# Kernel tuning notes

Measured on AMD Instinct MI355X. Metric: run time of the kernel, lower is better.

## Reference

```python
import jax, jax.numpy as jnp
import numpy as np

D, H, B = 512, 8, 64
NF, NO = 16384, 8192
EPS = 1e-5


def _ln(x):
    m = jnp.mean(x, axis=-1, keepdims=True)
    v = jnp.mean((x - m) ** 2, axis=-1, keepdims=True)
    return (x - m) / jnp.sqrt(v + EPS)


def setup_inputs() -> dict:
    key = jax.random.key(0)
    ks = jax.random.split(key, 16)
    s = 1.0 / np.sqrt(D)
    inp = {
        "hf": jax.random.normal(ks[0], (NF, D), jnp.float32),
        "ho": jax.random.normal(ks[1], (NO, D), jnp.float32),
        "ps": jax.random.normal(ks[2], (B, D), jnp.float32),
        "face_batch": jnp.sort(jax.random.randint(ks[3], (NF,), 0, B)),
        "obj_batch": jnp.sort(jax.random.randint(ks[4], (NO,), 0, B)),
        "Wq": jax.random.normal(ks[5], (D, D), jnp.float32) * s,
        "bq": jnp.zeros((D,), jnp.float32),
        "Wk": jax.random.normal(ks[6], (D, D), jnp.float32) * s,
        "bk": jnp.zeros((D,), jnp.float32),
        "Wv": jax.random.normal(ks[7], (D, D), jnp.float32) * s,
        "bv": jnp.zeros((D,), jnp.float32),
        "Wo": jax.random.normal(ks[8], (D, D), jnp.float32) * s,
        "bo": jnp.zeros((D,), jnp.float32),
        "Wg": jax.random.normal(ks[9], (D, D), jnp.float32) * s,
        "bg": jnp.full((D,), -1.0, jnp.float32),  # init.constant_(bias, -1.0)
        "alpha": jax.random.normal(ks[10], (D,), jnp.float32) * 0.1,
    }
    return inp


def reference(hf, ho, ps, face_batch, obj_batch, Wq, bq, Wk, bk, Wv, bv, Wo, bo, Wg, bg, alpha):
    dh = D // H
    nodes = jnp.concatenate([hf, ho], axis=0)            # (N, D)
    seg = jnp.concatenate([face_batch, obj_batch], 0)    # (N,)
    N = nodes.shape[0]

    # single-query cross-attention done as ragged/segment attention
    # (identical math to padded MHA with key_padding_mask)
    q = (ps @ Wq + bq).reshape(B, H, dh)                 # (B, H, dh)
    k = (nodes @ Wk + bk).reshape(N, H, dh)
    v = (nodes @ Wv + bv).reshape(N, H, dh)

    scores = jnp.einsum("nhd,nhd->nh", k, q[seg]) / np.sqrt(dh)   # (N, H)
    mx = jax.ops.segment_max(scores, seg, num_segments=B)          # (B, H)
    e = jnp.exp(scores - mx[seg])                                  # (N, H)
    denom = jax.ops.segment_sum(e, seg, num_segments=B)            # (B, H)
    num = jax.ops.segment_sum(e[:, :, None] * v, seg, num_segments=B)  # (B, H, dh)
    attn = (num / denom[:, :, None]).reshape(B, D)
    attn_out = attn @ Wo + bo

    fs = _ln(ps + attn_out)                               # (B, D)
    gate = jax.nn.sigmoid(hf @ Wg + bg)                   # (NF, D)
    signal = alpha * fs[face_batch]                       # (NF, D)
    hf_new = _ln(hf + gate * signal)
    return hf_new, fs
```

## Files before the change

### kernel.cpp

```cpp
#include <hip/hip_runtime.h>
#include <hip/hip_bf16.h>
#include <math.h>

constexpr int D  = 512;
constexpr int H  = 8;
constexpr int DH = 64;
constexpr int B  = 64;
constexpr int NF = 16384;
constexpr int NO = 8192;
constexpr int NT = NF + NO;
constexpr float EPS = 1e-5f;
constexpr float LOG2E = 1.4426950408889634f;

constexpr int PREP_PK   = 512;
constexpr int PREP_BND  = PREP_PK;
constexpr int PREP_WG0  = PREP_BND + 1;
constexpr int PREP_CVT0 = PREP_WG0 + 256;
constexpr int CVT_BLOCKS = NT * D / 2048;
constexpr int PREP_TOTAL = PREP_CVT0 + CVT_BLOCKS;

typedef short short8 __attribute__((ext_vector_type(8)));
typedef float f32x4 __attribute__((ext_vector_type(4)));
typedef unsigned short ushort;
typedef ushort ushort8v __attribute__((ext_vector_type(8)));

__device__ __forceinline__ ushort f2bf(float f) {
  unsigned int x = __float_as_uint(f);
  x += 0x7FFF + ((x >> 16) & 1);
  return (ushort)(x >> 16);
}
__device__ __forceinline__ float bf2f(ushort u) {
  return __uint_as_float(((unsigned int)u) << 16);
}
__device__ __forceinline__ float fast_exp(float x) {
  return __builtin_amdgcn_exp2f(x * LOG2E);
}
__device__ __forceinline__ float fast_sigmoid(float z) {
  return __builtin_amdgcn_rcpf(1.0f + __builtin_amdgcn_exp2f(-z * LOG2E));
}
__device__ __forceinline__ short8 cvt8(float4 f0, float4 f1) {
  union { short8 v; __hip_bfloat162 h[4]; } u;
  u.h[0] = __float22bfloat162_rn(float2{f0.x, f0.y});
  u.h[1] = __float22bfloat162_rn(float2{f0.z, f0.w});
  u.h[2] = __float22bfloat162_rn(float2{f1.x, f1.y});
  u.h[3] = __float22bfloat162_rn(float2{f1.z, f1.w});
  return u.v;
}
__device__ __forceinline__ void gll16(const void* g, void* l) {
  __builtin_amdgcn_global_load_lds(
      (const __attribute__((address_space(1))) void*)g,
      (__attribute__((address_space(3))) void*)l, 16, 0, 0);
}

__global__ __launch_bounds__(256) void k_prep(const float* __restrict__ ps,
                                              const float* __restrict__ Wq,
                                              const float* __restrict__ bq,
                                              const float* __restrict__ Wk,
                                              const float* __restrict__ bk,
                                              const float* __restrict__ Wg,
                                              const float* __restrict__ hf,
                                              const float* __restrict__ ho,
                                              const int* __restrict__ fb,
                                              const int* __restrict__ ob,
                                              float* __restrict__ Pk,
                                              float* __restrict__ qbk,
                                              ushort* __restrict__ Wgt,
                                              ushort* __restrict__ nodesb,
                                              int* __restrict__ fstart,
                                              int* __restrict__ ostart) {
  __shared__ float shm[1056];
  const int bid = blockIdx.x, t = threadIdx.x;
  if (bid < PREP_PK) {
    const int b = bid >> 3, h = bid & 7;
    for (int i = t; i < D; i += 256) shm[i] = ps[(size_t)b * D + i];
    __syncthreads();
    {
      const int j = t >> 2, eq = t & 3;
      const int col = h * 64 + j;
      float acc = 0.f;
      const float* wp = Wq + (size_t)(eq * 128) * D + col;
      #pragma unroll 8
      for (int e = 0; e < 128; ++e) acc += shm[eq * 128 + e] * wp[(size_t)e * D];
      acc += __shfl_xor(acc, 1); acc += __shfl_xor(acc, 2);
      if (eq == 0) shm[512 + j] = acc + bq[col];
    }
    __syncthreads();
    for (int e = t; e < D; e += 256) {
      float acc = 0.f;
      #pragma unroll 8
      for (int j = 0; j < DH; ++j) acc += Wk[(size_t)e * D + h * DH + j] * shm[512 + j];
      Pk[((size_t)b * H + h) * D + e] = acc;
    }
    if (t == 0) {
      float s = 0.f;
      for (int j = 0; j < DH; ++j) s += bk[h * DH + j] * shm[512 + j];
      qbk[b * H + h] = s;
    }
  } else if (bid == PREP_BND) {
    if (t <= B) {
      int lo = 0, hi = NF;
      while (lo < hi) { int mid = (lo + hi) >> 1; if (fb[mid] < t) lo = mid + 1; else hi = mid; }
      fstart[t] = lo;
    } else if (t >= 128 && t <= 128 + B) {
      int v = t - 128;
      int lo = 0, hi = NO;
      while (lo < hi) { int mid = (lo + hi) >> 1; if (ob[mid] < v) lo = mid + 1; else hi = mid; }
      ostart[v] = lo;
    }
  } else if (bid < PREP_CVT0) {
    float (*tile)[33] = (float(*)[33])shm;
    const int tb = bid - PREP_WG0;
    const int bx = tb & 15, by = tb >> 4;
    const int tx = t & 31, ty = t >> 5;
    #pragma unroll
    for (int i = 0; i < 4; ++i)
      tile[ty + i * 8][tx] = Wg[(size_t)(by * 32 + ty + i * 8) * D + bx * 32 + tx];
    __syncthreads();
    #pragma unroll
    for (int i = 0; i < 4; ++i)
      Wgt[(size_t)(bx * 32 + ty + i * 8) * D + by * 32 + tx] = f2bf(tile[tx][ty + i * 8]);
  } else {
    size_t idx = (size_t)(bid - PREP_CVT0) * 2048 + (size_t)t * 8;
    const float* src = (idx < (size_t)NF * D) ? (hf + idx) : (ho + (idx - (size_t)NF * D));
    float4 f0 = *(const float4*)src, f1 = *(const float4*)(src + 4);
    *(short8*)(nodesb + idx) = cvt8(f0, f1);
  }
}

__global__ __launch_bounds__(256) void k_gate(const ushort* __restrict__ hfb,
                                              const ushort* __restrict__ Wgt,
                                              const float* __restrict__ bg,
                                              ushort* __restrict__ gateb) {
  __shared__ ushort Asb[2][4096];
  __shared__ ushort Bs[2][4096];
  const int tid = threadIdx.x, lane = tid & 63, w = tid >> 6;
  const int rowBase = blockIdx.x * 128, colBase = blockIdx.y * 128;
  const int wm = w >> 1, wn = w & 1;
  const int lrow = lane & 15, kg = lane >> 4;

  int ra[2], ca[2], cb[2], cc[2];
  #pragma unroll
  for (int j = 0; j < 2; ++j) {
    int ia = (w * 2 + j) * 64 + lane;
    ra[j] = ia >> 2;
    ca[j] = (ia & 3) ^ ((ra[j] >> 1) & 3);
    cb[j] = ra[j];
    cc[j] = ca[j];
  }

#define STAGE(buf, k0)                                                          \
  {                                                                             \
    _Pragma("unroll")                                                           \
    for (int j = 0; j < 2; ++j)                                                 \
      gll16(hfb + (size_t)(rowBase + ra[j]) * D + (k0) + ca[j] * 8,             \
            &Asb[buf][(w * 2 + j) * 512]);                                      \
    _Pragma("unroll")                                                           \
    for (int j = 0; j < 2; ++j)                                                 \
      gll16(Wgt + (size_t)(colBase + cb[j]) * D + (k0) + cc[j] * 8,             \
            &Bs[buf][(w * 2 + j) * 512]);                                       \
  }

  STAGE(0, 0);
  __syncthreads();

  f32x4 acc[4][4] = {};
  for (int t = 0; t < 16; ++t) {
    const int cur = t & 1;
    if (t < 15) STAGE(cur ^ 1, (t + 1) * 32);
    short8 av[4], bv[4];
    #pragma unroll
    for (int m = 0; m < 4; ++m) {
      const int a_r = wm * 64 + m * 16 + lrow;
      av[m] = *(const short8*)&Asb[cur][a_r * 32 + (kg ^ ((a_r >> 1) & 3)) * 8];
    }
    #pragma unroll
    for (int n = 0; n < 4; ++n) {
      const int b_c = wn * 64 + n * 16 + lrow;
      bv[n] = *(const short8*)&Bs[cur][b_c * 32 + (kg ^ ((b_c >> 1) & 3)) * 8];
    }
    #pragma unroll
    for (int m = 0; m < 4; ++m)
      #pragma unroll
      for (int n = 0; n < 4; ++n)
        acc[m][n] = __builtin_amdgcn_mfma_f32_16x16x32_bf16(av[m], bv[n], acc[m][n], 0, 0, 0);
    __syncthreads();
  }
#undef STAGE

  #pragma unroll
  for (int n = 0; n < 4; ++n) {
    const int col = colBase + wn * 64 + n * 16 + lrow;
    const float bgv = bg[col];
    #pragma unroll
    for (int m = 0; m < 4; ++m) {
      const int row0 = rowBase + wm * 64 + m * 16 + kg * 4;
      #pragma unroll
      for (int r = 0; r < 4; ++r)
        gateb[(size_t)(row0 + r) * D + col] = f2bf(fast_sigmoid(acc[m][n][r] + bgv));
    }
  }
}

__global__ __launch_bounds__(256) void k_scores(const ushort* __restrict__ nodesb,
                                                const int* __restrict__ fb,
                                                const int* __restrict__ ob,
                                                const float* __restrict__ Pk,
                                                const float* __restrict__ qbk,
                                                float* __restrict__ scores) {
  int lane = threadIdx.x & 63;
  int n = blockIdx.x * 4 + (threadIdx.x >> 6);
  int b = (n < NF) ? fb[n] : ob[n - NF];
  union { short8 v; ushort u[8]; } ux;
  ux.v = *(const short8*)(nodesb + (size_t)n * D + lane * 8);
  float xf[8];
  #pragma unroll
  for (int i = 0; i < 8; ++i) xf[i] = bf2f(ux.u[i]);
  float acc[H];
  #pragma unroll
  for (int h = 0; h < H; ++h) {
    const float4* p4 = (const float4*)(Pk + ((size_t)b * H + h) * D) + lane * 2;
    float4 p0 = p4[0], p1 = p4[1];
    acc[h] = xf[0] * p0.x + xf[1] * p0.y + xf[2] * p0.z + xf[3] * p0.w +
             xf[4] * p1.x + xf[5] * p1.y + xf[6] * p1.z + xf[7] * p1.w;
  }
  #pragma unroll
  for (int h = 0; h < H; ++h) {
    float v = acc[h];
    #pragma unroll
    for (int off = 32; off; off >>= 1) v += __shfl_xor(v, off);
    if (lane == h) scores[(size_t)n * H + h] = (v + qbk[b * H + h]) * 0.125f;
  }
}

__global__ __launch_bounds__(512) void k_segsoftmax(const float* __restrict__ scores,
                                                    const int* __restrict__ fstart,
                                                    const int* __restrict__ ostart,
                                                    float* __restrict__ evals,
                                                    float* __restrict__ denom) {
  int b = blockIdx.x;
  int h = threadIdx.x >> 6, lane = threadIdx.x & 63;
  int f0 = fstart[b], f1 = fstart[b + 1];
  int o0 = ostart[b], o1 = ostart[b + 1];
  float m = -1e30f;
  for (int i = f0 + lane; i < f1; i += 64) m = fmaxf(m, scores[(size_t)i * H + h]);
  for (int i = o0 + lane; i < o1; i += 64) m = fmaxf(m, scores[(size_t)(NF + i) * H + h]);
  #pragma unroll
  for (int off = 32; off; off >>= 1) m = fmaxf(m, __shfl_xor(m, off));
  float s = 0.f;
  for (int i = f0 + lane; i < f1; i += 64) {
    float e = fast_exp(scores[(size_t)i * H + h] - m);
    evals[(size_t)i * H + h] = e; s += e;
  }
  for (int i = o0 + lane; i < o1; i += 64) {
    float e = fast_exp(scores[(size_t)(NF + i) * H + h] - m);
    evals[(size_t)(NF + i) * H + h] = e; s += e;
  }
  #pragma unroll
  for (int off = 32; off; off >>= 1) s += __shfl_xor(s, off);
  if (lane == 0) denom[b * H + h] = s;
}

__global__ __launch_bounds__(512) void k_Taccum(const ushort* __restrict__ nodesb,
                                                const int* __restrict__ fstart,
                                                const int* __restrict__ ostart,
                                                const float* __restrict__ evals,
                                                float* __restrict__ T8) {
  int b = blockIdx.x, chunk = blockIdx.y;
  int e = threadIdx.x;
  int f0 = fstart[b], flen = fstart[b + 1] - f0;
  int o0 = ostart[b], olen = ostart[b + 1] - o0;
  int L = flen + olen;
  float acc[8] = {0.f, 0.f, 0.f, 0.f, 0.f, 0.f, 0.f, 0.f};
  for (int idx = chunk; idx < L; idx += 8) {
    int n = (idx < flen) ? (f0 + idx) : (NF + o0 + (idx - flen));
    float x = bf2f(nodesb[(size_t)n * D + e]);
    const float4* ev = (const float4*)(evals + (size_t)n * H);
    float4 e0 = ev[0], e1 = ev[1];
    acc[0] += e0.x * x; acc[1] += e0.y * x; acc[2] += e0.z * x; acc[3] += e0.w * x;
    acc[4] += e1.x * x; acc[5] += e1.y * x; acc[6] += e1.z * x; acc[7] += e1.w * x;
  }
  #pragma unroll
  for (int h = 0; h < H; ++h)
    T8[(((size_t)chunk * B + b) * H + h) * D + e] = acc[h];
}

__global__ __launch_bounds__(256) void k_attn(const float* __restrict__ T8,
                                              const float* __restrict__ denom,
                                              const float* __restrict__ Wv,
                                              const float* __restrict__ bv,
                                              float* __restrict__ attn) {
  __shared__ float Ts[D];
  int b = blockIdx.x, h = blockIdx.y, t = threadIdx.x;
  for (int i = t; i < D; i += 256) {
    float s = 0.f;
    #pragma unroll
    for (int c2 = 0; c2 < 8; ++c2)
      s += T8[(((size_t)c2 * B + b) * H + h) * D + i];
    Ts[i] = s;
  }
  __syncthreads();
  int col = h * DH + (t >> 2), eq = t & 3;
  float acc = 0.f;
  const float* wp = Wv + (size_t)(eq * 128) * D + col;
  #pragma unroll 8
  for (int e = 0; e < 128; ++e) acc += Ts[eq * 128 + e] * wp[(size_t)e * D];
  acc += __shfl_xor(acc, 1); acc += __shfl_xor(acc, 2);
  if (eq == 0) attn[(size_t)b * D + col] = acc / denom[b * H + h] + bv[col];
}

__global__ __launch_bounds__(256) void k_x(const float* __restrict__ attn,
                                           const float* __restrict__ Wo,
                                           const float* __restrict__ bo,
                                           const float* __restrict__ ps,
                                           float* __restrict__ x) {
  __shared__ float As[D];
  int b = blockIdx.x, cg = blockIdx.y, t = threadIdx.x;
  for (int i = t; i < D; i += 256) As[i] = attn[(size_t)b * D + i];
  __syncthreads();
  int col = cg * 64 + (t >> 2), eq = t & 3;
  float acc = 0.f;
  const float* wp = Wo + (size_t)(eq * 128) * D + col;
  #pragma unroll 8
  for (int e = 0; e < 128; ++e) acc += As[eq * 128 + e] * wp[(size_t)e * D];
  acc += __shfl_xor(acc, 1); acc += __shfl_xor(acc, 2);
  if (eq == 0) x[(size_t)b * D + col] = acc + bo[col] + ps[(size_t)b * D + col];
}

__global__ __launch_bounds__(512) void k_ln(const float* __restrict__ x,
                                            float* __restrict__ fs) {
  __shared__ float redS[8], redQ[8];
  __shared__ float sM, sI;
  int b = blockIdx.x, t = threadIdx.x;
  float v = x[(size_t)b * D + t];
  float s = v, sq = v * v;
  #pragma unroll
  for (int off = 32; off; off >>= 1) { s += __shfl_xor(s, off); sq += __shfl_xor(sq, off); }
  int wv = t >> 6, ln = t & 63;
  if (ln == 0) { redS[wv] = s; redQ[wv] = sq; }
  __syncthreads();
  if (t == 0) {
    float S = 0.f, Q = 0.f;
    #pragma unroll
    for (int i = 0; i < 8; ++i) { S += redS[i]; Q += redQ[i]; }
    float mean = S * (1.f / D);
    float var = Q * (1.f / D) - mean * mean;
    sM = mean; sI = rsqrtf(var + EPS);
  }
  __syncthreads();
  fs[(size_t)b * D + t] = (v - sM) * sI;
}

__global__ __launch_bounds__(256) void k_final(const float* __restrict__ hf,
                                               const ushort* __restrict__ gateb,
                                               const float* __restrict__ alpha,
                                               const float* __restrict__ fs,
                                               const int* __restrict__ fb,
                                               float* __restrict__ out) {
  const int w = threadIdx.x >> 6, lane = threadIdx.x & 63;
  const int row = blockIdx.x * 4 + w;
  const int b = fb[row];
  const float* hr = hf + (size_t)row * D + lane * 8;
  const ushort* gr = gateb + (size_t)row * D + lane * 8;
  const float* fr = fs + (size_t)b * D + lane * 8;
  const float* ar = alpha + lane * 8;
  float4 h0 = *(const float4*)hr, h1 = *(const float4*)(hr + 4);
  union { ushort8v v; ushort u[8]; } ug;
  ug.v = *(const ushort8v*)gr;
  float4 p0 = *(const float4*)fr, p1 = *(const float4*)(fr + 4);
  float4 a0 = *(const float4*)ar, a1 = *(const float4*)(ar + 4);
  float hv[8] = {h0.x, h0.y, h0.z, h0.w, h1.x, h1.y, h1.z, h1.w};
  float pv[8] = {p0.x, p0.y, p0.z, p0.w, p1.x, p1.y, p1.z, p1.w};
  float av[8] = {a0.x, a0.y, a0.z, a0.w, a1.x, a1.y, a1.z, a1.w};
  float x[8], s = 0.f, sq = 0.f;
  #pragma unroll
  for (int i = 0; i < 8; ++i) {
    x[i] = hv[i] + bf2f(ug.u[i]) * (av[i] * pv[i]);
    s += x[i]; sq += x[i] * x[i];
  }
  #pragma unroll
  for (int off = 32; off; off >>= 1) { s += __shfl_xor(s, off); sq += __shfl_xor(sq, off); }
  float mean = s * (1.f / D);
  float inv = rsqrtf(sq * (1.f / D) - mean * mean + EPS);
  float* op = out + (size_t)row * D + lane * 8;
  float4 o0 = {(x[0] - mean) * inv, (x[1] - mean) * inv, (x[2] - mean) * inv, (x[3] - mean) * inv};
  float4 o1 = {(x[4] - mean) * inv, (x[5] - mean) * inv, (x[6] - mean) * inv, (x[7] - mean) * inv};
  *(float4*)op = o0;
  *(float4*)(op + 4) = o1;
}

extern "C" void kernel_launch(void* const* d_in, const int* in_sizes, int n_in,
                              void* d_out, int out_size, void* d_ws, size_t ws_size,
                              hipStream_t stream) {
  const float* hf    = (const float*)d_in[0];
  const float* ho    = (const float*)d_in[1];
  const float* ps    = (const float*)d_in[2];
  const int*   fb    = (const int*)d_in[3];
  const int*   ob    = (const int*)d_in[4];
  const float* Wq    = (const float*)d_in[5];
  const float* bq    = (const float*)d_in[6];
  const float* Wk    = (const float*)d_in[7];
  const float* bk    = (const float*)d_in[8];
  const float* Wv    = (const float*)d_in[9];
  const float* bv    = (const float*)d_in[10];
  const float* Wo    = (const float*)d_in[11];
  const float* bo    = (const float*)d_in[12];
  const float* Wg    = (const float*)d_in[13];
  const float* bg    = (const float*)d_in[14];
  const float* alpha = (const float*)d_in[15];

  float* out    = (float*)d_out;
  float* fs_out = out + (size_t)NF * D;

  ushort* Wgt    = (ushort*)d_ws;
  ushort* gateb  = Wgt + 512 * 512;
  ushort* nodesb = gateb + (size_t)NF * D;
  float* fbase   = (float*)(nodesb + (size_t)NT * D);
  float* Pk     = fbase;
  float* qbk    = Pk + B * H * D;
  float* scores = qbk + B * H;
  float* evals  = scores + (size_t)NT * H;
  float* denom  = evals + (size_t)NT * H;
  float* T8     = denom + B * H;
  float* attn   = T8 + (size_t)8 * B * H * D;
  float* xbuf   = attn + B * D;
  int* fstart   = (int*)(xbuf + B * D);
  int* ostart   = fstart + (B + 1);

  k_prep<<<PREP_TOTAL, 256, 0, stream>>>(ps, Wq, bq, Wk, bk, Wg, hf, ho, fb, ob,
                                         Pk, qbk, Wgt, nodesb, fstart, ostart);
  k_gate<<<dim3(NF / 128, 4), 256, 0, stream>>>(nodesb, Wgt, bg, gateb);
  k_scores<<<NT / 4, 256, 0, stream>>>(nodesb, fb, ob, Pk, qbk, scores);
  k_segsoftmax<<<B, 512, 0, stream>>>(scores, fstart, ostart, evals, denom);
  k_Taccum<<<dim3(B, 8), 512, 0, stream>>>(nodesb, fstart, ostart, evals, T8);
  k_attn<<<dim3(B, H), 256, 0, stream>>>(T8, denom, Wv, bv, attn);
  k_x<<<dim3(B, 8), 256, 0, stream>>>(attn, Wo, bo, ps, xbuf);
  k_ln<<<B, 512, 0, stream>>>(xbuf, fs_out);
  k_final<<<NF / 4, 256, 0, stream>>>(hf, gateb, alpha, fs_out, fb, out);
}
```

Before: 131.5 us.

## Stage Pk in LDS for scores, widen Taccum loads, read bf16 hf in final

```diff
diff --git a/kernel.cpp b/kernel.cpp
--- a/kernel.cpp
+++ b/kernel.cpp
@@ -207,21 +207,42 @@
                                                 const float* __restrict__ Pk,
                                                 const float* __restrict__ qbk,
                                                 float* __restrict__ scores) {
-  int lane = threadIdx.x & 63;
-  int n = blockIdx.x * 4 + (threadIdx.x >> 6);
-  int b = (n < NF) ? fb[n] : ob[n - NF];
+  __shared__ float Pks[H * D];
+  const int t = threadIdx.x, lane = t & 63;
+  const int n0 = blockIdx.x * 4;
+  const int b0 = (n0 < NF) ? fb[n0] : ob[n0 - NF];
+  {
+    const float4* src = (const float4*)(Pk + (size_t)b0 * H * D);
+    float4* dst = (float4*)Pks;
+    #pragma unroll
+    for (int i = 0; i < 4; ++i) dst[t + i * 256] = src[t + i * 256];
+  }
+  __syncthreads();
+
+  const int n = n0 + (t >> 6);
+  const int b = (n < NF) ? fb[n] : ob[n - NF];
   union { short8 v; ushort u[8]; } ux;
   ux.v = *(const short8*)(nodesb + (size_t)n * D + lane * 8);
   float xf[8];
   #pragma unroll
   for (int i = 0; i < 8; ++i) xf[i] = bf2f(ux.u[i]);
   float acc[H];
-  #pragma unroll
-  for (int h = 0; h < H; ++h) {
-    const float4* p4 = (const float4*)(Pk + ((size_t)b * H + h) * D) + lane * 2;
-    float4 p0 = p4[0], p1 = p4[1];
-    acc[h] = xf[0] * p0.x + xf[1] * p0.y + xf[2] * p0.z + xf[3] * p0.w +
-             xf[4] * p1.x + xf[5] * p1.y + xf[6] * p1.z + xf[7] * p1.w;
+  if (b == b0) {
+    #pragma unroll
+    for (int h = 0; h < H; ++h) {
+      const float4* p4 = (const float4*)(Pks + h * D + lane * 8);
+      float4 p0 = p4[0], p1 = p4[1];
+      acc[h] = xf[0] * p0.x + xf[1] * p0.y + xf[2] * p0.z + xf[3] * p0.w +
+               xf[4] * p1.x + xf[5] * p1.y + xf[6] * p1.z + xf[7] * p1.w;
+    }
+  } else {
+    #pragma unroll
+    for (int h = 0; h < H; ++h) {
+      const float4* p4 = (const float4*)(Pk + ((size_t)b * H + h) * D) + lane * 2;
+      float4 p0 = p4[0], p1 = p4[1];
+      acc[h] = xf[0] * p0.x + xf[1] * p0.y + xf[2] * p0.z + xf[3] * p0.w +
+               xf[4] * p1.x + xf[5] * p1.y + xf[6] * p1.z + xf[7] * p1.w;
+    }
   }
   #pragma unroll
   for (int h = 0; h < H; ++h) {
@@ -260,28 +281,38 @@
   if (lane == 0) denom[b * H + h] = s;
 }
 
-__global__ __launch_bounds__(512) void k_Taccum(const ushort* __restrict__ nodesb,
+__global__ __launch_bounds__(256) void k_Taccum(const ushort* __restrict__ nodesb,
                                                 const int* __restrict__ fstart,
                                                 const int* __restrict__ ostart,
                                                 const float* __restrict__ evals,
                                                 float* __restrict__ T8) {
   int b = blockIdx.x, chunk = blockIdx.y;
-  int e = threadIdx.x;
+  int e0 = threadIdx.x * 2;
   int f0 = fstart[b], flen = fstart[b + 1] - f0;
   int o0 = ostart[b], olen = ostart[b + 1] - o0;
   int L = flen + olen;
-  float acc[8] = {0.f, 0.f, 0.f, 0.f, 0.f, 0.f, 0.f, 0.f};
+  float acc0[8] = {0.f, 0.f, 0.f, 0.f, 0.f, 0.f, 0.f, 0.f};
+  float acc1[8] = {0.f, 0.f, 0.f, 0.f, 0.f, 0.f, 0.f, 0.f};
   for (int idx = chunk; idx < L; idx += 8) {
     int n = (idx < flen) ? (f0 + idx) : (NF + o0 + (idx - flen));
-    float x = bf2f(nodesb[(size_t)n * D + e]);
+    ushort2 uv = *(const ushort2*)(nodesb + (size_t)n * D + e0);
+    float x0 = bf2f(uv.x), x1 = bf2f(uv.y);
     const float4* ev = (const float4*)(evals + (size_t)n * H);
-    float4 e0 = ev[0], e1 = ev[1];
-    acc[0] += e0.x * x; acc[1] += e0.y * x; acc[2] += e0.z * x; acc[3] += e0.w * x;
-    acc[4] += e1.x * x; acc[5] += e1.y * x; acc[6] += e1.z * x; acc[7] += e1.w * x;
-  }
-  #pragma unroll
-  for (int h = 0; h < H; ++h)
-    T8[(((size_t)chunk * B + b) * H + h) * D + e] = acc[h];
+    float4 ea = ev[0], eb = ev[1];
+    acc0[0] += ea.x * x0; acc1[0] += ea.x * x1;
+    acc0[1] += ea.y * x0; acc1[1] += ea.y * x1;
+    acc0[2] += ea.z * x0; acc1[2] += ea.z * x1;
+    acc0[3] += ea.w * x0; acc1[3] += ea.w * x1;
+    acc0[4] += eb.x * x0; acc1[4] += eb.x * x1;
+    acc0[5] += eb.y * x0; acc1[5] += eb.y * x1;
+    acc0[6] += eb.z * x0; acc1[6] += eb.z * x1;
+    acc0[7] += eb.w * x0; acc1[7] += eb.w * x1;
+  }
+  #pragma unroll
+  for (int h = 0; h < H; ++h) {
+    float2 o = {acc0[h], acc1[h]};
+    *(float2*)&T8[(((size_t)chunk * B + b) * H + h) * D + e0] = o;
+  }
 }
 
 __global__ __launch_bounds__(256) void k_attn(const float* __restrict__ T8,
@@ -350,7 +381,7 @@
   fs[(size_t)b * D + t] = (v - sM) * sI;
 }
 
-__global__ __launch_bounds__(256) void k_final(const float* __restrict__ hf,
+__global__ __launch_bounds__(256) void k_final(const ushort* __restrict__ hfb,
                                                const ushort* __restrict__ gateb,
                                                const float* __restrict__ alpha,
                                                const float* __restrict__ fs,
@@ -359,22 +390,21 @@
   const int w = threadIdx.x >> 6, lane = threadIdx.x & 63;
   const int row = blockIdx.x * 4 + w;
   const int b = fb[row];
-  const float* hr = hf + (size_t)row * D + lane * 8;
+  const ushort* hr = hfb + (size_t)row * D + lane * 8;
   const ushort* gr = gateb + (size_t)row * D + lane * 8;
   const float* fr = fs + (size_t)b * D + lane * 8;
   const float* ar = alpha + lane * 8;
-  float4 h0 = *(const float4*)hr, h1 = *(const float4*)(hr + 4);
-  union { ushort8v v; ushort u[8]; } ug;
+  union { ushort8v v; ushort u[8]; } uh, ug;
+  uh.v = *(const ushort8v*)hr;
   ug.v = *(const ushort8v*)gr;
   float4 p0 = *(const float4*)fr, p1 = *(const float4*)(fr + 4);
   float4 a0 = *(const float4*)ar, a1 = *(const float4*)(ar + 4);
-  float hv[8] = {h0.x, h0.y, h0.z, h0.w, h1.x, h1.y, h1.z, h1.w};
   float pv[8] = {p0.x, p0.y, p0.z, p0.w, p1.x, p1.y, p1.z, p1.w};
   float av[8] = {a0.x, a0.y, a0.z, a0.w, a1.x, a1.y, a1.z, a1.w};
   float x[8], s = 0.f, sq = 0.f;
   #pragma unroll
   for (int i = 0; i < 8; ++i) {
-    x[i] = hv[i] + bf2f(ug.u[i]) * (av[i] * pv[i]);
+    x[i] = bf2f(uh.u[i]) + bf2f(ug.u[i]) * (av[i] * pv[i]);
     s += x[i]; sq += x[i] * x[i];
   }
   #pragma unroll
@@ -431,9 +461,9 @@
   k_gate<<<dim3(NF / 128, 4), 256, 0, stream>>>(nodesb, Wgt, bg, gateb);
   k_scores<<<NT / 4, 256, 0, stream>>>(nodesb, fb, ob, Pk, qbk, scores);
   k_segsoftmax<<<B, 512, 0, stream>>>(scores, fstart, ostart, evals, denom);
-  k_Taccum<<<dim3(B, 8), 512, 0, stream>>>(nodesb, fstart, ostart, evals, T8);
+  k_Taccum<<<dim3(B, 8), 256, 0, stream>>>(nodesb, fstart, ostart, evals, T8);
   k_attn<<<dim3(B, H), 256, 0, stream>>>(T8, denom, Wv, bv, attn);
   k_x<<<dim3(B, 8), 256, 0, stream>>>(attn, Wo, bo, ps, xbuf);
   k_ln<<<B, 512, 0, stream>>>(xbuf, fs_out);
-  k_final<<<NF / 4, 256, 0, stream>>>(hf, gateb, alpha, fs_out, fb, out);
-}
+  k_final<<<NF / 4, 256, 0, stream>>>(nodesb, gateb, alpha, fs_out, fb, out);
+}
```

New measurement: 134.3 us. 1.02x slower.
